# Kernel optimization log

Hardware: AMD Instinct MI355X
Metric: run time of the kernel (lower is better)

The kernel has to match this reference:

```python
import jax, jax.numpy as jnp
import numpy as np

N_NODES = 40000
N_EDGES = 640000
D_IN = 128
D_HID = 128
D_OUT = 128
N_GRAPHS = 128


def setup_inputs() -> dict:
    key = jax.random.key(0)
    ks = jax.random.split(key, 12)
    x = jax.random.normal(ks[0], (N_NODES, D_IN), dtype=jnp.float32)
    edge_index = jax.random.randint(ks[1], (2, N_EDGES), 0, N_NODES, dtype=jnp.int64)
    batch = jnp.sort(jax.random.randint(ks[2], (N_NODES,), 0, N_GRAPHS, dtype=jnp.int64))
    def lin(k, fan_in, shape):
        s = 1.0 / np.sqrt(fan_in)
        return jax.random.uniform(k, shape, dtype=jnp.float32, minval=-s, maxval=s)
    return {
        "x": x, "edge_index": edge_index, "batch": batch,
        "W_rel0": lin(ks[3], D_IN, (D_IN, D_HID)), "b_rel0": lin(ks[4], D_IN, (D_HID,)), "W_root0": lin(ks[5], D_IN, (D_IN, D_HID)),
        "W_rel1": lin(ks[6], D_HID, (D_HID, D_HID)), "b_rel1": lin(ks[7], D_HID, (D_HID,)), "W_root1": lin(ks[8], D_HID, (D_HID, D_HID)),
        "W_rel2": lin(ks[9], D_HID, (D_HID, D_OUT)), "b_rel2": lin(ks[10], D_HID, (D_OUT,)), "W_root2": lin(ks[11], D_HID, (D_HID, D_OUT)),
    }


def graph_conv(x, src, dst, W_rel, b_rel, W_root):
    # PyG GraphConv: out_i = Lin_rel(sum_{j in N(i)} x_j) + Lin_root(x_i)
    agg = jax.ops.segment_sum(x[src], dst, num_segments=N_NODES)  # [N, F]
    return agg @ W_rel + b_rel + x @ W_root


def reference(x, edge_index, batch,
              W_rel0, b_rel0, W_root0,
              W_rel1, b_rel1, W_root1,
              W_rel2, b_rel2, W_root2):
    src, dst = edge_index[0], edge_index[1]
    h = graph_conv(x, src, dst, W_rel0, b_rel0, W_root0)
    h = jax.nn.relu(h)  # dropout is identity in eval mode
    h = graph_conv(h, src, dst, W_rel1, b_rel1, W_root1)
    h = jax.nn.relu(h)
    h = graph_conv(h, src, dst, W_rel2, b_rel2, W_root2)
    # global_max_pool over per-node graph ids -> [n_graphs, D_OUT]
    return jax.ops.segment_max(h, batch, num_segments=N_GRAPHS)
```

## Files before the change

### kernel.cpp

```cpp
#include <hip/hip_runtime.h>
#include <hip/hip_bf16.h>
#include <math.h>

#define N_NODES 40000
#define N_EDGES 640000
#define D 128
#define N_GRAPHS 128
#define SCAN_NBLK ((N_NODES + 255) / 256)
#define LDS_STRIDE 68

typedef __attribute__((ext_vector_type(8))) short bf16x8;
typedef __attribute__((ext_vector_type(4))) float f32x4;
typedef __attribute__((ext_vector_type(2))) float f32x2;
typedef __attribute__((ext_vector_type(4))) unsigned int u32x4;
typedef __attribute__((ext_vector_type(2))) unsigned int u32x2;
typedef unsigned int __attribute__((address_space(3))) lds_u32;
typedef unsigned int __attribute__((address_space(1))) glb_u32;

static __device__ __forceinline__ unsigned short f2b(float f) {
    unsigned int u = __float_as_uint(f);
    unsigned int r = (u + 0x7fffu + ((u >> 16) & 1u)) >> 16;
    return (unsigned short)r;
}
static __device__ __forceinline__ unsigned int fkey(float x) {
    unsigned int b = __float_as_uint(x);
    return (b & 0x80000000u) ? ~b : (b | 0x80000000u);
}
static __device__ __forceinline__ unsigned int f2p8(float f) {
    return __builtin_amdgcn_cvt_pk_fp8_f32(f, 0.f, 0, false) & 0xffu;
}

__global__ void __launch_bounds__(256) k_init(
    int* __restrict__ counts,
    unsigned short* __restrict__ xb, unsigned short* __restrict__ hA,
    unsigned short* __restrict__ hB,
    unsigned char* __restrict__ x8, unsigned char* __restrict__ h8A,
    unsigned char* __restrict__ h8B, unsigned int* __restrict__ outk) {
    int n = blockIdx.x * 256 + threadIdx.x;
    if (n < N_GRAPHS * D) outk[n] = 0x007FFFFFu;
    if (n < N_NODES) counts[n] = 0;
    if (blockIdx.x == SCAN_NBLK) {
        int t = threadIdx.x;
        u32x4 z = {0u, 0u, 0u, 0u};
        if (t < 48) {
            int row = t >> 4, c = t & 15;
            unsigned short* p = (row == 0) ? xb : (row == 1) ? hA : hB;
            ((u32x4*)(p + (size_t)N_NODES * D))[c] = z;
        } else if (t < 72) {
            int row = (t - 48) >> 3, c = (t - 48) & 7;
            unsigned char* p = (row == 0) ? x8 : (row == 1) ? h8A : h8B;
            ((u32x4*)(p + (size_t)N_NODES * D))[c] = z;
        }
    }
}

__global__ void __launch_bounds__(256) k_pack1(
    const int* __restrict__ ei, int* __restrict__ counts,
    const float* __restrict__ x, unsigned int* __restrict__ xb,
    unsigned char* __restrict__ x8,
    const float* __restrict__ Wr0, const float* __restrict__ Wt0,
    const float* __restrict__ Wr1, const float* __restrict__ Wt1,
    const float* __restrict__ Wr2, const float* __restrict__ Wt2,
    unsigned short* __restrict__ WT) {
    int b = blockIdx.x;
    int t = threadIdx.x;
    if (b < 2500) {
        int e = b * 256 + t;
        atomicAdd(&counts[ei[N_EDGES + e]], 1);
    } else if (b < 5000) {
        int i = (b - 2500) * 256 + t;
        const f32x4* xv = (const f32x4*)x;
        f32x4 v0 = xv[i * 2], v1 = xv[i * 2 + 1];
        u32x4 o;
        o.x = ((unsigned int)f2b(v0.y) << 16) | f2b(v0.x);
        o.y = ((unsigned int)f2b(v0.w) << 16) | f2b(v0.z);
        o.z = ((unsigned int)f2b(v1.y) << 16) | f2b(v1.x);
        o.w = ((unsigned int)f2b(v1.w) << 16) | f2b(v1.z);
        ((u32x4*)xb)[i] = o;
        unsigned p0 = __builtin_amdgcn_cvt_pk_fp8_f32(v0.x, v0.y, 0, false);
        p0 = __builtin_amdgcn_cvt_pk_fp8_f32(v0.z, v0.w, p0, true);
        unsigned p1 = __builtin_amdgcn_cvt_pk_fp8_f32(v1.x, v1.y, 0, false);
        p1 = __builtin_amdgcn_cvt_pk_fp8_f32(v1.z, v1.w, p1, true);
        u32x2 o8; o8.x = p0; o8.y = p1;
        ((u32x2*)x8)[i] = o8;
    } else {
        int bw = b - 5000;
        int l = bw >> 7, c = bw & 127, k = t;
        const float* Wrel = (l == 0) ? Wr0 : (l == 1) ? Wr1 : Wr2;
        const float* Wroot = (l == 0) ? Wt0 : (l == 1) ? Wt1 : Wt2;
        float v = (k < D) ? Wrel[k * D + c] : Wroot[(k - D) * D + c];
        WT[(size_t)l * 128 * 256 + c * 256 + k] = f2b(v);
    }
}

__global__ void __launch_bounds__(256) k_scan1(const int* __restrict__ counts,
                                               int* __restrict__ local_pre,
                                               int* __restrict__ blocksums) {
    int t = threadIdx.x;
    int i = blockIdx.x * 256 + t;
    int lane = t & 63, wave = t >> 6;
    int v = (i < N_NODES) ? ((counts[i] + 15) & ~15) : 0;
    int incl = v;
#pragma unroll
    for (int off = 1; off < 64; off <<= 1) {
        int u = __shfl_up(incl, off);
        if (lane >= off) incl += u;
    }
    __shared__ int ws[4];
    if (lane == 63) ws[wave] = incl;
    __syncthreads();
    int base = 0;
    for (int w = 0; w < 4; ++w) {
        int s = ws[w];
        if (w < wave) base += s;
    }
    if (i < N_NODES) local_pre[i] = base + incl - v;
    if (t == 255) blocksums[blockIdx.x] = base + incl;
}

__global__ void __launch_bounds__(256) k_scan3(const int* __restrict__ local_pre,
                                               const int* __restrict__ blocksums,
                                               const int* __restrict__ counts,
                                               int* __restrict__ rp_pad,
                                               int* __restrict__ cursor,
                                               int* __restrict__ src_pad) {
    int t = threadIdx.x;
    int lane = t & 63, wave = t >> 6;
    int bid = blockIdx.x;
    int v = (t < bid) ? blocksums[t] : 0;
#pragma unroll
    for (int off = 32; off >= 1; off >>= 1) v += __shfl_xor(v, off);
    __shared__ int ws[4];
    if (lane == 0) ws[wave] = v;
    __syncthreads();
    int base = ws[0] + ws[1] + ws[2] + ws[3];

    int i = bid * 256 + t;
    if (i < N_NODES) {
        int rp = base + local_pre[i];
        rp_pad[i] = rp;
        cursor[i] = rp;
        int c = counts[i];
        int pc = (c + 15) & ~15;
        for (int j = rp + c; j < rp + pc; ++j) src_pad[j] = N_NODES;
        if (i == N_NODES - 1) rp_pad[N_NODES] = rp + pc;
    }
}

__global__ void k_scatter(const int* __restrict__ ei, int* __restrict__ cursor,
                          int* __restrict__ src_pad) {
    int e = blockIdx.x * blockDim.x + threadIdx.x;
    if (e < N_EDGES) {
        int d = ei[N_EDGES + e];
        int pos = atomicAdd(&cursor[d], 1);
        src_pad[pos] = ei[e];
    }
}

__global__ void __launch_bounds__(256) k_layer(
    const unsigned short* __restrict__ in,
    const unsigned char* __restrict__ in8,
    const int* __restrict__ rp_pad,
    const int* __restrict__ src_pad,
    const unsigned short* __restrict__ WT,
    const float* __restrict__ bias,
    unsigned short* __restrict__ out,
    unsigned char* __restrict__ out8,
    const int* __restrict__ batch,
    unsigned int* __restrict__ outk) {
    __shared__ __align__(1024) char stage[4][2][2048];
    __shared__ __align__(16) unsigned int aggLDS[16 * LDS_STRIDE];

    int tid = threadIdx.x;
    int w = tid >> 6;
    int lane = tid & 63;
    int nodebase = blockIdx.x * 16;

    const int* rp = rp_pad + nodebase + w * 4;
    int r0 = rp[0], r1 = rp[1], r2 = rp[2], r3 = rp[3], r4 = rp[4];

    int hh = lane >> 4;
    int cc = lane & 15;
    int j8 = lane >> 3;
    const char* in8b = (const char*)in8;
    unsigned gofs8 = 16u * (unsigned)(lane & 7);

#define STAGE2(BI, IA, IB) do {                                                \
        __builtin_amdgcn_global_load_lds(                                      \
            (const glb_u32*)(in8b + (((size_t)(unsigned)(IA)) << 7) + gofs8),  \
            (lds_u32*)&stage[w][BI][0], 16, 0, 0);                             \
        __builtin_amdgcn_global_load_lds(                                      \
            (const glb_u32*)(in8b + (((size_t)(unsigned)(IB)) << 7) + gofs8),  \
            (lds_u32*)&stage[w][BI][1024], 16, 0, 0);                          \
    } while (0)

    int ia = 0, ib = 0;
    int pos = r0;
    int buf_i = 0, buf_c = 0;
    if (pos < r4) {
        ia = src_pad[pos + j8];
        ib = src_pad[pos + 8 + j8];
        STAGE2(0, ia, ib);
        buf_i = 1;
        pos += 16;
        if (pos < r4) {
            ia = src_pad[pos + j8];
            ib = src_pad[pos + 8 + j8];
        }
    }

#pragma unroll
    for (int n = 0; n < 4; ++n) {
        int ps = (n == 0) ? r0 : (n == 1) ? r1 : (n == 2) ? r2 : r3;
        int pe = (n == 0) ? r1 : (n == 1) ? r2 : (n == 2) ? r3 : r4;
        float a0 = 0.f, a1 = 0.f, a2 = 0.f, a3 = 0.f;
        float a4 = 0.f, a5 = 0.f, a6 = 0.f, a7 = 0.f;
        for (int p = ps; p < pe; p += 16) {
            asm volatile("s_waitcnt vmcnt(0)" ::: "memory");
            if (pos < r4) {
                STAGE2(buf_i, ia, ib);
                buf_i ^= 1;
                pos += 16;
                if (pos < r4) {
                    ia = src_pad[pos + j8];
                    ib = src_pad[pos + 8 + j8];
                }
            }
            const char* sb = &stage[w][buf_c][0];
#pragma unroll
            for (int pp = 0; pp < 4; ++pp) {
                u32x2 dv = *(const u32x2*)(sb + 512 * pp + 128 * hh + 8 * cc);
                f32x2 l0 = __builtin_amdgcn_cvt_pk_f32_fp8(dv.x, false);
                f32x2 h0 = __builtin_amdgcn_cvt_pk_f32_fp8(dv.x, true);
                f32x2 l1 = __builtin_amdgcn_cvt_pk_f32_fp8(dv.y, false);
                f32x2 h1 = __builtin_amdgcn_cvt_pk_f32_fp8(dv.y, true);
                a0 += l0.x; a1 += l0.y; a2 += h0.x; a3 += h0.y;
                a4 += l1.x; a5 += l1.y; a6 += h1.x; a7 += h1.y;
            }
            buf_c ^= 1;
        }
#define RED(a) do { a += __shfl_xor(a, 16); a += __shfl_xor(a, 32); } while (0)
        RED(a0); RED(a1); RED(a2); RED(a3);
        RED(a4); RED(a5); RED(a6); RED(a7);
#undef RED
        if (lane < 16) {
            u32x4 o;
            o.x = ((unsigned int)f2b(a1) << 16) | f2b(a0);
            o.y = ((unsigned int)f2b(a3) << 16) | f2b(a2);
            o.z = ((unsigned int)f2b(a5) << 16) | f2b(a4);
            o.w = ((unsigned int)f2b(a7) << 16) | f2b(a6);
            *(u32x4*)&aggLDS[(w * 4 + n) * LDS_STRIDE + 4 * cc] = o;
        }
    }
#undef STAGE2
    __syncthreads();

    int row = cc, quad = hh;
    int colbase = w * 32;

    f32x4 gacc0 = {0.f, 0.f, 0.f, 0.f};
    f32x4 gacc1 = {0.f, 0.f, 0.f, 0.f};

    const unsigned int* Al = &aggLDS[row * LDS_STRIDE];
    const short* Xp = (const short*)(in + (nodebase + row) * D);
    const short* W0 = (const short*)(WT + (colbase + row) * 256);
    const short* W1 = (const short*)(WT + (colbase + 16 + row) * 256);

#pragma unroll
    for (int t = 0; t < 4; ++t) {
        bf16x8 af = *(const bf16x8*)(Al + t * 16 + quad * 4);
        int k0 = t * 32 + quad * 8;
        bf16x8 b0 = *(const bf16x8*)(W0 + k0);
        bf16x8 b1 = *(const bf16x8*)(W1 + k0);
        gacc0 = __builtin_amdgcn_mfma_f32_16x16x32_bf16(af, b0, gacc0, 0, 0, 0);
        gacc1 = __builtin_amdgcn_mfma_f32_16x16x32_bf16(af, b1, gacc1, 0, 0, 0);
    }
#pragma unroll
    for (int t = 0; t < 4; ++t) {
        int k0 = t * 32 + quad * 8;
        bf16x8 xf = *(const bf16x8*)(Xp + k0);
        bf16x8 b0 = *(const bf16x8*)(W0 + 128 + k0);
        bf16x8 b1 = *(const bf16x8*)(W1 + 128 + k0);
        gacc0 = __builtin_amdgcn_mfma_f32_16x16x32_bf16(xf, b0, gacc0, 0, 0, 0);
        gacc1 = __builtin_amdgcn_mfma_f32_16x16x32_bf16(xf, b1, gacc1, 0, 0, 0);
    }

    int c0 = colbase + row, c1 = c0 + 16;
    float bia0 = bias[c0], bia1 = bias[c1];
    float v0[4], v1[4];
#pragma unroll
    for (int r = 0; r < 4; ++r) { v0[r] = gacc0[r] + bia0; v1[r] = gacc1[r] + bia1; }

    if (outk == nullptr) {
#pragma unroll
        for (int r = 0; r < 4; ++r) {
            int n2 = nodebase + quad * 4 + r;
            float r0v = fmaxf(v0[r], 0.f), r1v = fmaxf(v1[r], 0.f);
            out[n2 * D + c0] = f2b(r0v);
            out[n2 * D + c1] = f2b(r1v);
            v0[r] = r0v; v1[r] = r1v;
        }
        __syncthreads();
        unsigned char* agg8 = (unsigned char*)aggLDS;
#pragma unroll
        for (int r = 0; r < 4; ++r) {
            int n2l = quad * 4 + r;
            agg8[n2l * 128 + c0] = (unsigned char)f2p8(v0[r]);
            agg8[n2l * 128 + c1] = (unsigned char)f2p8(v1[r]);
        }
        __syncthreads();
        if (tid < 128) {
            int nl = tid >> 3, co = (tid & 7) * 16;
            *(u32x4*)(out8 + (size_t)(nodebase + nl) * D + co) =
                *(const u32x4*)(agg8 + nl * 128 + co);
        }
    } else {
        int g0 = batch[nodebase];
        int g15 = batch[nodebase + 15];
        if (g0 == g15) {
            float m0 = fmaxf(fmaxf(v0[0], v0[1]), fmaxf(v0[2], v0[3]));
            float m1 = fmaxf(fmaxf(v1[0], v1[1]), fmaxf(v1[2], v1[3]));
            m0 = fmaxf(m0, __shfl_xor(m0, 16)); m0 = fmaxf(m0, __shfl_xor(m0, 32));
            m1 = fmaxf(m1, __shfl_xor(m1, 16)); m1 = fmaxf(m1, __shfl_xor(m1, 32));
            if (quad == 0) {
                atomicMax(&outk[g0 * D + c0], fkey(m0));
                atomicMax(&outk[g0 * D + c1], fkey(m1));
            }
        } else {
#pragma unroll
            for (int r = 0; r < 4; ++r) {
                int gg = batch[nodebase + quad * 4 + r];
                atomicMax(&outk[gg * D + c0], fkey(v0[r]));
                atomicMax(&outk[gg * D + c1], fkey(v1[r]));
            }
        }
    }
}

__global__ void k_unmap(unsigned int* __restrict__ outk) {
    int i = blockIdx.x * 256 + threadIdx.x;
    unsigned int k = outk[i];
    unsigned int b = (k & 0x80000000u) ? (k ^ 0x80000000u) : ~k;
    ((float*)outk)[i] = __uint_as_float(b);
}

extern "C" void kernel_launch(void* const* d_in, const int* in_sizes, int n_in,
                              void* d_out, int out_size, void* d_ws, size_t ws_size,
                              hipStream_t stream) {
    const float* x = (const float*)d_in[0];
    const int* ei = (const int*)d_in[1];
    const int* batch = (const int*)d_in[2];
    const float* Wrel[3]  = {(const float*)d_in[3], (const float*)d_in[6], (const float*)d_in[9]};
    const float* brel[3]  = {(const float*)d_in[4], (const float*)d_in[7], (const float*)d_in[10]};
    const float* Wroot[3] = {(const float*)d_in[5], (const float*)d_in[8], (const float*)d_in[11]};
    unsigned int* outk = (unsigned int*)d_out;

    char* ws = (char*)d_ws;
    size_t off = 0;
    auto alloc = [&](size_t bytes) -> void* {
        void* p = ws + off;
        off = (off + bytes + 255) & ~(size_t)255;
        return p;
    };
    unsigned short* xb  = (unsigned short*)alloc((size_t)(N_NODES + 1) * D * 2);
    unsigned short* hA  = (unsigned short*)alloc((size_t)(N_NODES + 1) * D * 2);
    unsigned short* hB  = (unsigned short*)alloc((size_t)(N_NODES + 1) * D * 2);
    unsigned char* x8   = (unsigned char*)alloc((size_t)(N_NODES + 1) * D);
    unsigned char* h8A  = (unsigned char*)alloc((size_t)(N_NODES + 1) * D);
    unsigned char* h8B  = (unsigned char*)alloc((size_t)(N_NODES + 1) * D);
    unsigned short* WT  = (unsigned short*)alloc((size_t)3 * 128 * 256 * 2);
    int* rp_pad     = (int*)alloc((size_t)(N_NODES + 1) * 4);
    int* counts     = (int*)alloc((size_t)N_NODES * 4);
    int* cursor     = (int*)alloc((size_t)N_NODES * 4);
    int* src_pad    = (int*)alloc((size_t)(N_EDGES + 16 * N_NODES) * 4);
    int* local_pre  = (int*)alloc((size_t)N_NODES * 4);
    int* blocksums  = (int*)alloc((size_t)SCAN_NBLK * 4);

    k_init<<<SCAN_NBLK + 1, 256, 0, stream>>>(counts, xb, hA, hB, x8, h8A, h8B, outk);
    k_pack1<<<5384, 256, 0, stream>>>(ei, counts, x, (unsigned int*)xb, x8,
                                      Wrel[0], Wroot[0], Wrel[1], Wroot[1],
                                      Wrel[2], Wroot[2], WT);
    k_scan1<<<SCAN_NBLK, 256, 0, stream>>>(counts, local_pre, blocksums);
    k_scan3<<<SCAN_NBLK, 256, 0, stream>>>(local_pre, blocksums, counts,
                                           rp_pad, cursor, src_pad);
    k_scatter<<<(N_EDGES + 255) / 256, 256, 0, stream>>>(ei, cursor, src_pad);

    k_layer<<<N_NODES / 16, 256, 0, stream>>>(xb, x8, rp_pad, src_pad, WT,
                                              brel[0], hA, h8A, batch, nullptr);
    k_layer<<<N_NODES / 16, 256, 0, stream>>>(hA, h8A, rp_pad, src_pad, WT + 128 * 256,
                                              brel[1], hB, h8B, batch, nullptr);
    k_layer<<<N_NODES / 16, 256, 0, stream>>>(hB, h8B, rp_pad, src_pad, WT + 2 * 128 * 256,
                                              brel[2], hB, h8B, batch, outk);

    k_unmap<<<N_GRAPHS * D / 256, 256, 0, stream>>>(outk);
}
```

Measured before the change: 266.1 us.

## Replace LDS-staged gather with register-prefetched fp8 loads in layer kernel

The neighbour gather in the layer kernel no longer stages fp8 rows through LDS with global_load_lds and a full vmcnt(0) wait per chunk. Each wave now prefetches all its edge indices up front, broadcasts them with shuffles, and keeps four chunks of dwordx4 row loads in flight in registers, using graded vmcnt waits. The aggregate is reduced across lanes and packed to bf16 with v_cvt_pk_bf16_f32. Runs longer than 192 edges fall back to a simple unpipelined loop. This removes LDS staging traffic and serialised waits, at the cost of more registers and inline-asm fragility.

```diff
diff --git a/kernel.cpp b/kernel.cpp
--- a/kernel.cpp
+++ b/kernel.cpp
@@ -14,8 +14,6 @@
 typedef __attribute__((ext_vector_type(2))) float f32x2;
 typedef __attribute__((ext_vector_type(4))) unsigned int u32x4;
 typedef __attribute__((ext_vector_type(2))) unsigned int u32x2;
-typedef unsigned int __attribute__((address_space(3))) lds_u32;
-typedef unsigned int __attribute__((address_space(1))) glb_u32;
 
 static __device__ __forceinline__ unsigned short f2b(float f) {
     unsigned int u = __float_as_uint(f);
@@ -168,7 +166,6 @@
     unsigned char* __restrict__ out8,
     const int* __restrict__ batch,
     unsigned int* __restrict__ outk) {
-    __shared__ __align__(1024) char stage[4][2][2048];
     __shared__ __align__(16) unsigned int aggLDS[16 * LDS_STRIDE];
 
     int tid = threadIdx.x;
@@ -177,84 +174,142 @@
     int nodebase = blockIdx.x * 16;
 
     const int* rp = rp_pad + nodebase + w * 4;
-    int r0 = rp[0], r1 = rp[1], r2 = rp[2], r3 = rp[3], r4 = rp[4];
+    int r0 = __builtin_amdgcn_readfirstlane(rp[0]);
+    int r1 = __builtin_amdgcn_readfirstlane(rp[1]);
+    int r2 = __builtin_amdgcn_readfirstlane(rp[2]);
+    int r3 = __builtin_amdgcn_readfirstlane(rp[3]);
+    int r4 = __builtin_amdgcn_readfirstlane(rp[4]);
+
+    int j8 = lane >> 3;
+    unsigned long long base8 =
+        (unsigned long long)(const void*)in8 + 16u * (unsigned)(lane & 7);
+
+    float acc0 = 0.f, acc1 = 0.f, acc2 = 0.f, acc3 = 0.f;
+    float acc4 = 0.f, acc5 = 0.f, acc6 = 0.f, acc7 = 0.f;
+    float acc8 = 0.f, acc9 = 0.f, acc10 = 0.f, acc11 = 0.f;
+    float acc12 = 0.f, acc13 = 0.f, acc14 = 0.f, acc15 = 0.f;
+
+    auto cons1 = [&](u32x4 v) {
+        f32x2 p;
+        p = __builtin_amdgcn_cvt_pk_f32_fp8(v.x, false); acc0 += p.x; acc1 += p.y;
+        p = __builtin_amdgcn_cvt_pk_f32_fp8(v.x, true);  acc2 += p.x; acc3 += p.y;
+        p = __builtin_amdgcn_cvt_pk_f32_fp8(v.y, false); acc4 += p.x; acc5 += p.y;
+        p = __builtin_amdgcn_cvt_pk_f32_fp8(v.y, true);  acc6 += p.x; acc7 += p.y;
+        p = __builtin_amdgcn_cvt_pk_f32_fp8(v.z, false); acc8 += p.x; acc9 += p.y;
+        p = __builtin_amdgcn_cvt_pk_f32_fp8(v.z, true);  acc10 += p.x; acc11 += p.y;
+        p = __builtin_amdgcn_cvt_pk_f32_fp8(v.w, false); acc12 += p.x; acc13 += p.y;
+        p = __builtin_amdgcn_cvt_pk_f32_fp8(v.w, true);  acc14 += p.x; acc15 += p.y;
+    };
+    auto flushNode = [&](int ndv) {
+#define RZ(a) { a += __shfl_xor(a, 8); a += __shfl_xor(a, 16); a += __shfl_xor(a, 32); }
+        RZ(acc0) RZ(acc1) RZ(acc2) RZ(acc3)
+        RZ(acc4) RZ(acc5) RZ(acc6) RZ(acc7)
+        RZ(acc8) RZ(acc9) RZ(acc10) RZ(acc11)
+        RZ(acc12) RZ(acc13) RZ(acc14) RZ(acc15)
+#undef RZ
+        if (lane < 8) {
+            unsigned w0, w1, w2, w3, w4, w5, w6, w7;
+            asm("v_cvt_pk_bf16_f32 %0, %1, %2" : "=v"(w0) : "v"(acc0),  "v"(acc1));
+            asm("v_cvt_pk_bf16_f32 %0, %1, %2" : "=v"(w1) : "v"(acc2),  "v"(acc3));
+            asm("v_cvt_pk_bf16_f32 %0, %1, %2" : "=v"(w2) : "v"(acc4),  "v"(acc5));
+            asm("v_cvt_pk_bf16_f32 %0, %1, %2" : "=v"(w3) : "v"(acc6),  "v"(acc7));
+            asm("v_cvt_pk_bf16_f32 %0, %1, %2" : "=v"(w4) : "v"(acc8),  "v"(acc9));
+            asm("v_cvt_pk_bf16_f32 %0, %1, %2" : "=v"(w5) : "v"(acc10), "v"(acc11));
+            asm("v_cvt_pk_bf16_f32 %0, %1, %2" : "=v"(w6) : "v"(acc12), "v"(acc13));
+            asm("v_cvt_pk_bf16_f32 %0, %1, %2" : "=v"(w7) : "v"(acc14), "v"(acc15));
+            u32x4 q0 = {w0, w1, w2, w3};
+            u32x4 q1 = {w4, w5, w6, w7};
+            unsigned int* rowp = &aggLDS[(w * 4 + ndv) * LDS_STRIDE + 8 * lane];
+            *(u32x4*)rowp = q0;
+            *(u32x4*)(rowp + 4) = q1;
+        }
+        acc0 = acc1 = acc2 = acc3 = 0.f;
+        acc4 = acc5 = acc6 = acc7 = 0.f;
+        acc8 = acc9 = acc10 = acc11 = 0.f;
+        acc12 = acc13 = acc14 = acc15 = 0.f;
+    };
+
+    int run = r4 - r0;
+    if (run <= 192) {
+        int iv0, iv1, iv2;
+        {
+            unsigned long long ia =
+                (unsigned long long)(const void*)(src_pad + r0) + 4u * (unsigned)lane;
+            asm volatile(
+                "global_load_dword %0, %3, off\n\t"
+                "global_load_dword %1, %3, off offset:256\n\t"
+                "global_load_dword %2, %3, off offset:512\n\t"
+                "s_waitcnt vmcnt(0)"
+                : "=&v"(iv0), "=&v"(iv1), "=&v"(iv2)
+                : "v"(ia) : "memory");
+            __builtin_amdgcn_sched_barrier(0);
+        }
+        int E1 = (r1 - r0) >> 4, E2 = (r2 - r0) >> 4, E3 = (r3 - r0) >> 4;
+        int nch = run >> 4;
+        auto endOf = [&](int k) {
+            return k == 0 ? E1 : k == 1 ? E2 : k == 2 ? E3 : nch;
+        };
+        int nd = 0;
+        while (nd < 4 && endOf(nd) <= 0) { flushNode(nd); ++nd; }
+
+        u32x4 A0, B0, A1, B1, A2, B2, A3, B3;
+        auto issue = [&](u32x4& VA, u32x4& VB, int ivv, int c) {
+            int slotA = ((c * 16) & 63) + j8;
+            int rowA = __shfl(ivv, slotA);
+            int rowB = __shfl(ivv, slotA + 8);
+            unsigned long long aA = base8 + (unsigned long long)((unsigned)rowA << 7);
+            unsigned long long aB = base8 + (unsigned long long)((unsigned)rowB << 7);
+            asm volatile(
+                "global_load_dwordx4 %0, %2, off\n\t"
+                "global_load_dwordx4 %1, %3, off"
+                : "=&v"(VA), "=&v"(VB)
+                : "v"(aA), "v"(aB) : "memory");
+        };
+        if (nch > 0) issue(A0, B0, iv0, 0);
+        if (nch > 1) issue(A1, B1, iv0, 1);
+        if (nch > 2) issue(A2, B2, iv0, 2);
+        if (nch > 3) issue(A3, B3, iv0, 3);
+
+        for (int cb = 0; cb < nch; cb += 4) {
+            int ivnext = ((cb >> 2) == 0) ? iv1 : iv2;
+#define SUBSTEP(K, VA, VB) { int c = cb + K; if (c < nch) {                      \
+            int rem = nch - 1 - c;                                               \
+            if (rem > 2)       { asm volatile("s_waitcnt vmcnt(6)" ::: "memory"); } \
+            else if (rem == 2) { asm volatile("s_waitcnt vmcnt(4)" ::: "memory"); } \
+            else if (rem == 1) { asm volatile("s_waitcnt vmcnt(2)" ::: "memory"); } \
+            else               { asm volatile("s_waitcnt vmcnt(0)" ::: "memory"); } \
+            __builtin_amdgcn_sched_barrier(0);                                   \
+            cons1(VA); cons1(VB);                                                \
+            int done = c + 1;                                                    \
+            while (nd < 4 && endOf(nd) <= done) { flushNode(nd); ++nd; }         \
+            if (c + 4 < nch) issue(VA, VB, ivnext, c + 4); } }
+            SUBSTEP(0, A0, B0)
+            SUBSTEP(1, A1, B1)
+            SUBSTEP(2, A2, B2)
+            SUBSTEP(3, A3, B3)
+#undef SUBSTEP
+        }
+    } else {
+        const char* in8b = (const char*)in8;
+        int f16o = 16 * (lane & 7);
+        int ps = r0;
+        for (int ndv = 0; ndv < 4; ++ndv) {
+            int pe = (ndv == 0) ? r1 : (ndv == 1) ? r2 : (ndv == 2) ? r3 : r4;
+            for (int p = ps; p < pe; p += 16) {
+                int ia = src_pad[p + j8];
+                int ib = src_pad[p + 8 + j8];
+                u32x4 va = *(const u32x4*)(in8b + (((size_t)(unsigned)ia) << 7) + f16o);
+                u32x4 vb = *(const u32x4*)(in8b + (((size_t)(unsigned)ib) << 7) + f16o);
+                cons1(va); cons1(vb);
+            }
+            flushNode(ndv);
+            ps = pe;
+        }
+    }
+    __syncthreads();
 
     int hh = lane >> 4;
     int cc = lane & 15;
-    int j8 = lane >> 3;
-    const char* in8b = (const char*)in8;
-    unsigned gofs8 = 16u * (unsigned)(lane & 7);
-
-#define STAGE2(BI, IA, IB) do {                                                \
-        __builtin_amdgcn_global_load_lds(                                      \
-            (const glb_u32*)(in8b + (((size_t)(unsigned)(IA)) << 7) + gofs8),  \
-            (lds_u32*)&stage[w][BI][0], 16, 0, 0);                             \
-        __builtin_amdgcn_global_load_lds(                                      \
-            (const glb_u32*)(in8b + (((size_t)(unsigned)(IB)) << 7) + gofs8),  \
-            (lds_u32*)&stage[w][BI][1024], 16, 0, 0);                          \
-    } while (0)
-
-    int ia = 0, ib = 0;
-    int pos = r0;
-    int buf_i = 0, buf_c = 0;
-    if (pos < r4) {
-        ia = src_pad[pos + j8];
-        ib = src_pad[pos + 8 + j8];
-        STAGE2(0, ia, ib);
-        buf_i = 1;
-        pos += 16;
-        if (pos < r4) {
-            ia = src_pad[pos + j8];
-            ib = src_pad[pos + 8 + j8];
-        }
-    }
-
-#pragma unroll
-    for (int n = 0; n < 4; ++n) {
-        int ps = (n == 0) ? r0 : (n == 1) ? r1 : (n == 2) ? r2 : r3;
-        int pe = (n == 0) ? r1 : (n == 1) ? r2 : (n == 2) ? r3 : r4;
-        float a0 = 0.f, a1 = 0.f, a2 = 0.f, a3 = 0.f;
-        float a4 = 0.f, a5 = 0.f, a6 = 0.f, a7 = 0.f;
-        for (int p = ps; p < pe; p += 16) {
-            asm volatile("s_waitcnt vmcnt(0)" ::: "memory");
-            if (pos < r4) {
-                STAGE2(buf_i, ia, ib);
-                buf_i ^= 1;
-                pos += 16;
-                if (pos < r4) {
-                    ia = src_pad[pos + j8];
-                    ib = src_pad[pos + 8 + j8];
-                }
-            }
-            const char* sb = &stage[w][buf_c][0];
-#pragma unroll
-            for (int pp = 0; pp < 4; ++pp) {
-                u32x2 dv = *(const u32x2*)(sb + 512 * pp + 128 * hh + 8 * cc);
-                f32x2 l0 = __builtin_amdgcn_cvt_pk_f32_fp8(dv.x, false);
-                f32x2 h0 = __builtin_amdgcn_cvt_pk_f32_fp8(dv.x, true);
-                f32x2 l1 = __builtin_amdgcn_cvt_pk_f32_fp8(dv.y, false);
-                f32x2 h1 = __builtin_amdgcn_cvt_pk_f32_fp8(dv.y, true);
-                a0 += l0.x; a1 += l0.y; a2 += h0.x; a3 += h0.y;
-                a4 += l1.x; a5 += l1.y; a6 += h1.x; a7 += h1.y;
-            }
-            buf_c ^= 1;
-        }
-#define RED(a) do { a += __shfl_xor(a, 16); a += __shfl_xor(a, 32); } while (0)
-        RED(a0); RED(a1); RED(a2); RED(a3);
-        RED(a4); RED(a5); RED(a6); RED(a7);
-#undef RED
-        if (lane < 16) {
-            u32x4 o;
-            o.x = ((unsigned int)f2b(a1) << 16) | f2b(a0);
-            o.y = ((unsigned int)f2b(a3) << 16) | f2b(a2);
-            o.z = ((unsigned int)f2b(a5) << 16) | f2b(a4);
-            o.w = ((unsigned int)f2b(a7) << 16) | f2b(a6);
-            *(u32x4*)&aggLDS[(w * 4 + n) * LDS_STRIDE + 4 * cc] = o;
-        }
-    }
-#undef STAGE2
-    __syncthreads();
-
     int row = cc, quad = hh;
     int colbase = w * 32;
 
```

After: 284.9 us. 1.07x slower.

## Deepen gather pipeline to four LDS stages with LDS-staged edge indices

Applied to the files above, without the earlier changes.

The per-wave neighbour gather now loads up to 192 source indices into LDS in one shot and keeps three chunk loads in flight across a four-buffer ring. It waits with graded vmcnt counts instead of draining to zero every chunk. It also treats the four nodes' edges as one continuous chunk stream, flushing each node when its chunks finish. A fallback keeps the old double-buffered path for waves with more than 192 edges. The aim is to hide gather latency, at the cost of more LDS per block, which may lower occupancy.

```diff
diff --git a/kernel.cpp b/kernel.cpp
--- a/kernel.cpp
+++ b/kernel.cpp
@@ -168,7 +168,8 @@
     unsigned char* __restrict__ out8,
     const int* __restrict__ batch,
     unsigned int* __restrict__ outk) {
-    __shared__ __align__(1024) char stage[4][2][2048];
+    __shared__ __align__(1024) char stage[4][4][2048];
+    __shared__ int idxb[4][192];
     __shared__ __align__(16) unsigned int aggLDS[16 * LDS_STRIDE];
 
     int tid = threadIdx.x;
@@ -185,60 +186,31 @@
     const char* in8b = (const char*)in8;
     unsigned gofs8 = 16u * (unsigned)(lane & 7);
 
-#define STAGE2(BI, IA, IB) do {                                                \
-        __builtin_amdgcn_global_load_lds(                                      \
-            (const glb_u32*)(in8b + (((size_t)(unsigned)(IA)) << 7) + gofs8),  \
-            (lds_u32*)&stage[w][BI][0], 16, 0, 0);                             \
-        __builtin_amdgcn_global_load_lds(                                      \
-            (const glb_u32*)(in8b + (((size_t)(unsigned)(IB)) << 7) + gofs8),  \
-            (lds_u32*)&stage[w][BI][1024], 16, 0, 0);                          \
-    } while (0)
-
-    int ia = 0, ib = 0;
-    int pos = r0;
-    int buf_i = 0, buf_c = 0;
-    if (pos < r4) {
-        ia = src_pad[pos + j8];
-        ib = src_pad[pos + 8 + j8];
-        STAGE2(0, ia, ib);
-        buf_i = 1;
-        pos += 16;
-        if (pos < r4) {
-            ia = src_pad[pos + j8];
-            ib = src_pad[pos + 8 + j8];
-        }
-    }
-
-#pragma unroll
-    for (int n = 0; n < 4; ++n) {
-        int ps = (n == 0) ? r0 : (n == 1) ? r1 : (n == 2) ? r2 : r3;
-        int pe = (n == 0) ? r1 : (n == 1) ? r2 : (n == 2) ? r3 : r4;
-        float a0 = 0.f, a1 = 0.f, a2 = 0.f, a3 = 0.f;
-        float a4 = 0.f, a5 = 0.f, a6 = 0.f, a7 = 0.f;
-        for (int p = ps; p < pe; p += 16) {
-            asm volatile("s_waitcnt vmcnt(0)" ::: "memory");
-            if (pos < r4) {
-                STAGE2(buf_i, ia, ib);
-                buf_i ^= 1;
-                pos += 16;
-                if (pos < r4) {
-                    ia = src_pad[pos + j8];
-                    ib = src_pad[pos + 8 + j8];
-                }
-            }
-            const char* sb = &stage[w][buf_c][0];
-#pragma unroll
-            for (int pp = 0; pp < 4; ++pp) {
-                u32x2 dv = *(const u32x2*)(sb + 512 * pp + 128 * hh + 8 * cc);
-                f32x2 l0 = __builtin_amdgcn_cvt_pk_f32_fp8(dv.x, false);
-                f32x2 h0 = __builtin_amdgcn_cvt_pk_f32_fp8(dv.x, true);
-                f32x2 l1 = __builtin_amdgcn_cvt_pk_f32_fp8(dv.y, false);
-                f32x2 h1 = __builtin_amdgcn_cvt_pk_f32_fp8(dv.y, true);
-                a0 += l0.x; a1 += l0.y; a2 += h0.x; a3 += h0.y;
-                a4 += l1.x; a5 += l1.y; a6 += h1.x; a7 += h1.y;
-            }
-            buf_c ^= 1;
-        }
+    float a0 = 0.f, a1 = 0.f, a2 = 0.f, a3 = 0.f;
+    float a4 = 0.f, a5 = 0.f, a6 = 0.f, a7 = 0.f;
+
+    auto stg = [&](int bi, int ia2, int ib2) {
+        __builtin_amdgcn_global_load_lds(
+            (const glb_u32*)(in8b + (((size_t)(unsigned)ia2) << 7) + gofs8),
+            (lds_u32*)&stage[w][bi][0], 16, 0, 0);
+        __builtin_amdgcn_global_load_lds(
+            (const glb_u32*)(in8b + (((size_t)(unsigned)ib2) << 7) + gofs8),
+            (lds_u32*)&stage[w][bi][1024], 16, 0, 0);
+    };
+    auto unp = [&](int bi) {
+        const char* sb = &stage[w][bi][0];
+#pragma unroll
+        for (int pp = 0; pp < 4; ++pp) {
+            u32x2 dv = *(const u32x2*)(sb + 512 * pp + 128 * hh + 8 * cc);
+            f32x2 l0 = __builtin_amdgcn_cvt_pk_f32_fp8(dv.x, false);
+            f32x2 h0 = __builtin_amdgcn_cvt_pk_f32_fp8(dv.x, true);
+            f32x2 l1 = __builtin_amdgcn_cvt_pk_f32_fp8(dv.y, false);
+            f32x2 h1 = __builtin_amdgcn_cvt_pk_f32_fp8(dv.y, true);
+            a0 += l0.x; a1 += l0.y; a2 += h0.x; a3 += h0.y;
+            a4 += l1.x; a5 += l1.y; a6 += h1.x; a7 += h1.y;
+        }
+    };
+    auto flushNode = [&](int ndv) {
 #define RED(a) do { a += __shfl_xor(a, 16); a += __shfl_xor(a, 32); } while (0)
         RED(a0); RED(a1); RED(a2); RED(a3);
         RED(a4); RED(a5); RED(a6); RED(a7);
@@ -249,10 +221,92 @@
             o.y = ((unsigned int)f2b(a3) << 16) | f2b(a2);
             o.z = ((unsigned int)f2b(a5) << 16) | f2b(a4);
             o.w = ((unsigned int)f2b(a7) << 16) | f2b(a6);
-            *(u32x4*)&aggLDS[(w * 4 + n) * LDS_STRIDE + 4 * cc] = o;
-        }
-    }
-#undef STAGE2
+            *(u32x4*)&aggLDS[(w * 4 + ndv) * LDS_STRIDE + 4 * cc] = o;
+        }
+        a0 = a1 = a2 = a3 = 0.f;
+        a4 = a5 = a6 = a7 = 0.f;
+    };
+
+    int run = r4 - r0;
+    if (run <= 192) {
+        {
+            const int* sp = src_pad + r0;
+#pragma unroll
+            for (int k = 0; k < 3; ++k) {
+                __builtin_amdgcn_global_load_lds(
+                    (const glb_u32*)(sp + 64 * k + lane),
+                    (lds_u32*)&idxb[w][64 * k], 4, 0, 0);
+            }
+            asm volatile("s_waitcnt vmcnt(0)" ::: "memory");
+            __builtin_amdgcn_sched_barrier(0);
+        }
+        int nch = run >> 4;
+        int E1 = (r1 - r0) >> 4, E2 = (r2 - r0) >> 4, E3 = (r3 - r0) >> 4;
+        auto endOf = [&](int k) {
+            return k == 0 ? E1 : k == 1 ? E2 : k == 2 ? E3 : nch;
+        };
+        int nd = 0;
+        while (nd < 4 && endOf(nd) <= 0) { flushNode(nd); ++nd; }
+#pragma unroll
+        for (int k = 0; k < 3; ++k) {
+            if (k < nch) {
+                int ia = idxb[w][k * 16 + j8];
+                int ib = idxb[w][k * 16 + 8 + j8];
+                stg(k, ia, ib);
+            }
+        }
+        for (int c = 0; c < nch; ++c) {
+            if (c + 3 < nch) {
+                int ia = idxb[w][(c + 3) * 16 + j8];
+                int ib = idxb[w][(c + 3) * 16 + 8 + j8];
+                stg((c + 3) & 3, ia, ib);
+            }
+            int S = nch - 1 - c; if (S > 3) S = 3;
+            if (S == 3)      { asm volatile("s_waitcnt vmcnt(6)" ::: "memory"); }
+            else if (S == 2) { asm volatile("s_waitcnt vmcnt(4)" ::: "memory"); }
+            else if (S == 1) { asm volatile("s_waitcnt vmcnt(2)" ::: "memory"); }
+            else             { asm volatile("s_waitcnt vmcnt(0)" ::: "memory"); }
+            __builtin_amdgcn_sched_barrier(0);
+            unp(c & 3);
+            int done = c + 1;
+            while (nd < 4 && endOf(nd) <= done) { flushNode(nd); ++nd; }
+        }
+    } else {
+        int ia = 0, ib = 0;
+        int pos = r0;
+        int bi = 0, bc = 0;
+        if (pos < r4) {
+            ia = src_pad[pos + j8];
+            ib = src_pad[pos + 8 + j8];
+            stg(0, ia, ib);
+            bi = 1;
+            pos += 16;
+            if (pos < r4) {
+                ia = src_pad[pos + j8];
+                ib = src_pad[pos + 8 + j8];
+            }
+        }
+#pragma unroll
+        for (int n = 0; n < 4; ++n) {
+            int ps = (n == 0) ? r0 : (n == 1) ? r1 : (n == 2) ? r2 : r3;
+            int pe = (n == 0) ? r1 : (n == 1) ? r2 : (n == 2) ? r3 : r4;
+            for (int p = ps; p < pe; p += 16) {
+                asm volatile("s_waitcnt vmcnt(0)" ::: "memory");
+                if (pos < r4) {
+                    stg(bi, ia, ib);
+                    bi ^= 1;
+                    pos += 16;
+                    if (pos < r4) {
+                        ia = src_pad[pos + j8];
+                        ib = src_pad[pos + 8 + j8];
+                    }
+                }
+                unp(bc);
+                bc ^= 1;
+            }
+            flushNode(n);
+        }
+    }
     __syncthreads();
 
     int row = cc, quad = hh;
```

Measured after the change: 290.4 us. 1.09x slower.

## Split fused layer into two half-width gather kernels plus separate GEMM kernel

Applied to the files above, without the earlier changes.

The fused gather+GEMM layer kernel is split into k_gather (templated on which 64-byte half of each fp8 row to fetch) and k_gemm, with the aggregate round-tripping through a global bf16 buffer. Each gather pass touches only half of every source row, likely to improve cache hit rates on the random neighbour gather. The cost is two extra launches per layer and an extra global write and read of the aggregate. The last layer now writes its bf16 output through a null pointer unless the outk branch skips that store.

```diff
diff --git a/kernel.cpp b/kernel.cpp
--- a/kernel.cpp
+++ b/kernel.cpp
@@ -7,7 +7,6 @@
 #define D 128
 #define N_GRAPHS 128
 #define SCAN_NBLK ((N_NODES + 255) / 256)
-#define LDS_STRIDE 68
 
 typedef __attribute__((ext_vector_type(8))) short bf16x8;
 typedef __attribute__((ext_vector_type(4))) float f32x4;
@@ -157,119 +156,123 @@
     }
 }
 
-__global__ void __launch_bounds__(256) k_layer(
-    const unsigned short* __restrict__ in,
+template <int HALF>
+__global__ void __launch_bounds__(256) k_gather(
     const unsigned char* __restrict__ in8,
     const int* __restrict__ rp_pad,
     const int* __restrict__ src_pad,
+    unsigned short* __restrict__ aggG) {
+    __shared__ __align__(1024) char stage[4][2][1024];
+
+    int tid = threadIdx.x;
+    int w = tid >> 6;
+    int lane = tid & 63;
+    int nodebase = blockIdx.x * 16;
+
+    const int* rp = rp_pad + nodebase + w * 4;
+    int r0 = rp[0], r1 = rp[1], r2 = rp[2], r3 = rp[3], r4 = rp[4];
+
+    int j16 = lane >> 2;
+    unsigned q16 = (unsigned)(lane & 3) * 16u;
+    int j8 = lane >> 3;
+    int c8 = lane & 7;
+    const char* in8b = (const char*)in8;
+
+    float a0 = 0.f, a1 = 0.f, a2 = 0.f, a3 = 0.f;
+    float a4 = 0.f, a5 = 0.f, a6 = 0.f, a7 = 0.f;
+
+#define STAGE1(BI, IA)                                                         \
+    __builtin_amdgcn_global_load_lds(                                          \
+        (const glb_u32*)(in8b + (((size_t)(unsigned)(IA)) << 7) +              \
+                         (HALF ? 64u : 0u) + q16),                             \
+        (lds_u32*)&stage[w][BI][0], 16, 0, 0)
+
+    auto acc2 = [&](u32x2 dv) {
+        f32x2 p;
+        p = __builtin_amdgcn_cvt_pk_f32_fp8(dv.x, false); a0 += p.x; a1 += p.y;
+        p = __builtin_amdgcn_cvt_pk_f32_fp8(dv.x, true);  a2 += p.x; a3 += p.y;
+        p = __builtin_amdgcn_cvt_pk_f32_fp8(dv.y, false); a4 += p.x; a5 += p.y;
+        p = __builtin_amdgcn_cvt_pk_f32_fp8(dv.y, true);  a6 += p.x; a7 += p.y;
+    };
+
+    int ia = 0;
+    int pos = r0;
+    int bi = 0, bc = 0;
+    if (pos < r4) {
+        ia = src_pad[pos + j16];
+        STAGE1(0, ia);
+        bi = 1;
+        pos += 16;
+        if (pos < r4) ia = src_pad[pos + j16];
+    }
+
+#pragma unroll
+    for (int n = 0; n < 4; ++n) {
+        int ps = (n == 0) ? r0 : (n == 1) ? r1 : (n == 2) ? r2 : r3;
+        int pe = (n == 0) ? r1 : (n == 1) ? r2 : (n == 2) ? r3 : r4;
+        for (int p = ps; p < pe; p += 16) {
+            asm volatile("s_waitcnt vmcnt(0)" ::: "memory");
+            if (pos < r4) {
+                STAGE1(bi, ia);
+                bi ^= 1;
+                pos += 16;
+                if (pos < r4) ia = src_pad[pos + j16];
+            }
+            const char* sb = &stage[w][bc][0];
+            u32x2 d0 = *(const u32x2*)(sb + j8 * 64 + c8 * 8);
+            u32x2 d1 = *(const u32x2*)(sb + (j8 + 8) * 64 + c8 * 8);
+            acc2(d0);
+            acc2(d1);
+            bc ^= 1;
+        }
+#define RZ(a) { a += __shfl_xor(a, 8); a += __shfl_xor(a, 16); a += __shfl_xor(a, 32); }
+        RZ(a0) RZ(a1) RZ(a2) RZ(a3) RZ(a4) RZ(a5) RZ(a6) RZ(a7)
+#undef RZ
+        if (lane < 8) {
+            u32x4 o;
+            o.x = ((unsigned int)f2b(a1) << 16) | f2b(a0);
+            o.y = ((unsigned int)f2b(a3) << 16) | f2b(a2);
+            o.z = ((unsigned int)f2b(a5) << 16) | f2b(a4);
+            o.w = ((unsigned int)f2b(a7) << 16) | f2b(a6);
+            *(u32x4*)(aggG + (size_t)(nodebase + w * 4 + n) * D +
+                      (HALF ? 64 : 0) + c8 * 8) = o;
+        }
+        a0 = a1 = a2 = a3 = 0.f;
+        a4 = a5 = a6 = a7 = 0.f;
+    }
+#undef STAGE1
+}
+
+__global__ void __launch_bounds__(256) k_gemm(
+    const unsigned short* __restrict__ in,
+    const unsigned short* __restrict__ aggG,
     const unsigned short* __restrict__ WT,
     const float* __restrict__ bias,
     unsigned short* __restrict__ out,
     unsigned char* __restrict__ out8,
     const int* __restrict__ batch,
     unsigned int* __restrict__ outk) {
-    __shared__ __align__(1024) char stage[4][2][2048];
-    __shared__ __align__(16) unsigned int aggLDS[16 * LDS_STRIDE];
+    __shared__ unsigned char agg8[16 * 128];
 
     int tid = threadIdx.x;
     int w = tid >> 6;
     int lane = tid & 63;
     int nodebase = blockIdx.x * 16;
-
-    const int* rp = rp_pad + nodebase + w * 4;
-    int r0 = rp[0], r1 = rp[1], r2 = rp[2], r3 = rp[3], r4 = rp[4];
-
-    int hh = lane >> 4;
-    int cc = lane & 15;
-    int j8 = lane >> 3;
-    const char* in8b = (const char*)in8;
-    unsigned gofs8 = 16u * (unsigned)(lane & 7);
-
-#define STAGE2(BI, IA, IB) do {                                                \
-        __builtin_amdgcn_global_load_lds(                                      \
-            (const glb_u32*)(in8b + (((size_t)(unsigned)(IA)) << 7) + gofs8),  \
-            (lds_u32*)&stage[w][BI][0], 16, 0, 0);                             \
-        __builtin_amdgcn_global_load_lds(                                      \
-            (const glb_u32*)(in8b + (((size_t)(unsigned)(IB)) << 7) + gofs8),  \
-            (lds_u32*)&stage[w][BI][1024], 16, 0, 0);                          \
-    } while (0)
-
-    int ia = 0, ib = 0;
-    int pos = r0;
-    int buf_i = 0, buf_c = 0;
-    if (pos < r4) {
-        ia = src_pad[pos + j8];
-        ib = src_pad[pos + 8 + j8];
-        STAGE2(0, ia, ib);
-        buf_i = 1;
-        pos += 16;
-        if (pos < r4) {
-            ia = src_pad[pos + j8];
-            ib = src_pad[pos + 8 + j8];
-        }
-    }
-
-#pragma unroll
-    for (int n = 0; n < 4; ++n) {
-        int ps = (n == 0) ? r0 : (n == 1) ? r1 : (n == 2) ? r2 : r3;
-        int pe = (n == 0) ? r1 : (n == 1) ? r2 : (n == 2) ? r3 : r4;
-        float a0 = 0.f, a1 = 0.f, a2 = 0.f, a3 = 0.f;
-        float a4 = 0.f, a5 = 0.f, a6 = 0.f, a7 = 0.f;
-        for (int p = ps; p < pe; p += 16) {
-            asm volatile("s_waitcnt vmcnt(0)" ::: "memory");
-            if (pos < r4) {
-                STAGE2(buf_i, ia, ib);
-                buf_i ^= 1;
-                pos += 16;
-                if (pos < r4) {
-                    ia = src_pad[pos + j8];
-                    ib = src_pad[pos + 8 + j8];
-                }
-            }
-            const char* sb = &stage[w][buf_c][0];
-#pragma unroll
-            for (int pp = 0; pp < 4; ++pp) {
-                u32x2 dv = *(const u32x2*)(sb + 512 * pp + 128 * hh + 8 * cc);
-                f32x2 l0 = __builtin_amdgcn_cvt_pk_f32_fp8(dv.x, false);
-                f32x2 h0 = __builtin_amdgcn_cvt_pk_f32_fp8(dv.x, true);
-                f32x2 l1 = __builtin_amdgcn_cvt_pk_f32_fp8(dv.y, false);
-                f32x2 h1 = __builtin_amdgcn_cvt_pk_f32_fp8(dv.y, true);
-                a0 += l0.x; a1 += l0.y; a2 += h0.x; a3 += h0.y;
-                a4 += l1.x; a5 += l1.y; a6 += h1.x; a7 += h1.y;
-            }
-            buf_c ^= 1;
-        }
-#define RED(a) do { a += __shfl_xor(a, 16); a += __shfl_xor(a, 32); } while (0)
-        RED(a0); RED(a1); RED(a2); RED(a3);
-        RED(a4); RED(a5); RED(a6); RED(a7);
-#undef RED
-        if (lane < 16) {
-            u32x4 o;
-            o.x = ((unsigned int)f2b(a1) << 16) | f2b(a0);
-            o.y = ((unsigned int)f2b(a3) << 16) | f2b(a2);
-            o.z = ((unsigned int)f2b(a5) << 16) | f2b(a4);
-            o.w = ((unsigned int)f2b(a7) << 16) | f2b(a6);
-            *(u32x4*)&aggLDS[(w * 4 + n) * LDS_STRIDE + 4 * cc] = o;
-        }
-    }
-#undef STAGE2
-    __syncthreads();
-
-    int row = cc, quad = hh;
+    int row = lane & 15, quad = lane >> 4;
     int colbase = w * 32;
 
     f32x4 gacc0 = {0.f, 0.f, 0.f, 0.f};
     f32x4 gacc1 = {0.f, 0.f, 0.f, 0.f};
 
-    const unsigned int* Al = &aggLDS[row * LDS_STRIDE];
-    const short* Xp = (const short*)(in + (nodebase + row) * D);
+    const short* Ap = (const short*)(aggG + (size_t)(nodebase + row) * D);
+    const short* Xp = (const short*)(in + (size_t)(nodebase + row) * D);
     const short* W0 = (const short*)(WT + (colbase + row) * 256);
     const short* W1 = (const short*)(WT + (colbase + 16 + row) * 256);
 
 #pragma unroll
     for (int t = 0; t < 4; ++t) {
-        bf16x8 af = *(const bf16x8*)(Al + t * 16 + quad * 4);
         int k0 = t * 32 + quad * 8;
+        bf16x8 af = *(const bf16x8*)(Ap + k0);
         bf16x8 b0 = *(const bf16x8*)(W0 + k0);
         bf16x8 b1 = *(const bf16x8*)(W1 + k0);
         gacc0 = __builtin_amdgcn_mfma_f32_16x16x32_bf16(af, b0, gacc0, 0, 0, 0);
@@ -300,8 +303,6 @@
             out[n2 * D + c1] = f2b(r1v);
             v0[r] = r0v; v1[r] = r1v;
         }
-        __syncthreads();
-        unsigned char* agg8 = (unsigned char*)aggLDS;
 #pragma unroll
         for (int r = 0; r < 4; ++r) {
             int n2l = quad * 4 + r;
@@ -368,6 +369,7 @@
     unsigned char* x8   = (unsigned char*)alloc((size_t)(N_NODES + 1) * D);
     unsigned char* h8A  = (unsigned char*)alloc((size_t)(N_NODES + 1) * D);
     unsigned char* h8B  = (unsigned char*)alloc((size_t)(N_NODES + 1) * D);
+    unsigned short* aggG = (unsigned short*)alloc((size_t)N_NODES * D * 2);
     unsigned short* WT  = (unsigned short*)alloc((size_t)3 * 128 * 256 * 2);
     int* rp_pad     = (int*)alloc((size_t)(N_NODES + 1) * 4);
     int* counts     = (int*)alloc((size_t)N_NODES * 4);
@@ -385,12 +387,17 @@
                                            rp_pad, cursor, src_pad);
     k_scatter<<<(N_EDGES + 255) / 256, 256, 0, stream>>>(ei, cursor, src_pad);
 
-    k_layer<<<N_NODES / 16, 256, 0, stream>>>(xb, x8, rp_pad, src_pad, WT,
-                                              brel[0], hA, h8A, batch, nullptr);
-    k_layer<<<N_NODES / 16, 256, 0, stream>>>(hA, h8A, rp_pad, src_pad, WT + 128 * 256,
-                                              brel[1], hB, h8B, batch, nullptr);
-    k_layer<<<N_NODES / 16, 256, 0, stream>>>(hB, h8B, rp_pad, src_pad, WT + 2 * 128 * 256,
-                                              brel[2], hB, h8B, batch, outk);
+    const unsigned char* in8s[3] = {x8, h8A, h8B};
+    const unsigned short* ins[3] = {xb, hA, hB};
+    unsigned short* outs[3] = {hA, hB, nullptr};
+    unsigned char* out8s[3] = {h8A, h8B, nullptr};
+    for (int l = 0; l < 3; ++l) {
+        k_gather<0><<<N_NODES / 16, 256, 0, stream>>>(in8s[l], rp_pad, src_pad, aggG);
+        k_gather<1><<<N_NODES / 16, 256, 0, stream>>>(in8s[l], rp_pad, src_pad, aggG);
+        k_gemm<<<N_NODES / 16, 256, 0, stream>>>(ins[l], aggG, WT + l * 128 * 256,
+                                                 brel[l], outs[l], out8s[l], batch,
+                                                 (l == 2) ? outk : nullptr);
+    }
 
     k_unmap<<<N_GRAPHS * D / 256, 256, 0, stream>>>(outk);
 }
```

After: 345.0 us. 29.6% more time.
